# Optimization experiments

Hardware: AMD Instinct MI355X
Metric: run time of the kernel (lower is better)

The kernel has to match this reference:

```python
import jax, jax.numpy as jnp
import numpy as np

B, L, D, N_ORIG, GD, K_TARGET = 8, 512, 1024, 8192, 64, 256
_PI, _PJ = np.triu_indices(L, k=1)  # all global pairs i<j, shared across batch


def setup_inputs() -> dict:
    key = jax.random.key(0)
    k1, k2, k3 = jax.random.split(key, 3)
    x = jax.random.normal(k1, (B, L, D), jnp.float32)
    source = jax.random.uniform(k2, (B, L, N_ORIG), jnp.float32)
    W = jax.random.normal(k3, (GD, D), jnp.float32) * 0.02  # group_proj weight (out,in), no bias
    return {"x": x, "source": source, "W": W, "target_len": K_TARGET}


def _merge_single(x, s, W, r_step, pi, pj):
    # x: (S,D), s: (S,N). One greedy global merge step (r_step = S//2 >= r_total).
    S = x.shape[0]
    g = x @ W.T                                   # (S, GD)
    gn = jnp.linalg.norm(g, axis=-1)              # token weights (g.norm)
    gu = g / jnp.maximum(gn, 1e-12)[:, None]      # F.normalize(g, dim=-1)
    sim = (gu[pi] * gu[pj]).sum(-1)               # (P,) cosine sim of each pair
    # deterministic order: (-sim, i, j); lexsort's last key is primary
    order = jnp.lexsort((pj, pi, -sim))
    si = pi[order]
    sj = pj[order]

    # sequential greedy disjoint (mutual-exclusion) selection
    def body(carry, ij):
        partner, isj, cnt = carry
        i, j = ij
        used_i = (partner[i] >= 0) | isj[i]
        used_j = (partner[j] >= 0) | isj[j]
        sel = (~used_i) & (~used_j) & (cnt < r_step)
        partner = partner.at[i].set(jnp.where(sel, j, partner[i]))
        isj = isj.at[j].set(isj[j] | sel)
        return (partner, isj, cnt + sel.astype(jnp.int32)), None

    init = (jnp.full((S,), -1, jnp.int32), jnp.zeros((S,), bool), jnp.int32(0))
    (partner, isj, _), _ = jax.lax.scan(body, init, (si, sj))

    # kept tokens (everything not a merged-away j), in original order; greedy on a
    # complete graph always selects exactly r_step pairs, so K = S - r_step is static
    K = S - r_step
    keep = jnp.argsort(isj.astype(jnp.int32), stable=True)[:K]  # (K,)
    pk = partner[keep]
    has_p = pk >= 0
    pjx = jnp.where(has_p, pk, keep)  # safe partner index
    wi = gn[keep]
    wj = gn[pjx]
    tot = wi + wj + 1e-8
    xm = jnp.where(has_p[:, None], (wi[:, None] * x[keep] + wj[:, None] * x[pjx]) / tot[:, None], x[keep])
    sm = jnp.where(has_p[:, None], s[keep] + s[pjx], s[keep])
    return xm, sm


def reference(x, source, W, target_len):
    Bb, Ll, Dd = x.shape
    r_total = Ll - target_len
    if r_total <= 0:
        return x, source
    # with target_len = L//2, r_total <= floor(L/2): single greedy step (faithful)
    r_step = min(r_total, Ll // 2)
    pi = jnp.asarray(_PI, jnp.int32)
    pj = jnp.asarray(_PJ, jnp.int32)
    f = lambda xb, sb: _merge_single(xb, sb, W, r_step, pi, pj)
    return jax.vmap(f)(x, source)
```

## Files before the change

### kernel.cpp

```cpp
#include <hip/hip_runtime.h>

#define B_ 8
#define L_ 512
#define D_ 1024
#define N_ 8192
#define GD_ 64
#define K_ 256

#define XQ(q) ((q) ^ (((q) >> 4) & 7))

__global__ __launch_bounds__(256) void wt_kernel(const float* __restrict__ W,
                                                 float* __restrict__ Wt) {
  int idx = blockIdx.x * 256 + threadIdx.x;
  int d = idx >> 6, g = idx & 63;
  Wt[idx] = W[(size_t)g * D_ + d];
}

__global__ __launch_bounds__(256) void gproj_kernel(const float* __restrict__ x,
                                                    const float* __restrict__ Wt,
                                                    float* __restrict__ gu,
                                                    float* __restrict__ gn) {
  __shared__ __align__(16) float xs[16 * 1024];
  __shared__ __align__(16) float red[16][16][64];
  int blk = blockIdx.x;
  int b = blk >> 5;
  int t0 = (blk & 31) * 16;
  int tid = threadIdx.x;
  const float* xb = x + ((size_t)b * L_ + t0) * D_;
  for (int r = 0; r < 16; ++r) {
    int idx = r * 256 + tid;
    int tok = idx >> 8, q = idx & 255;
    float4 v = *(const float4*)(xb + (size_t)tok * D_ + q * 4);
    *(float4*)&xs[tok * 1024 + XQ(q) * 4] = v;
  }
  __syncthreads();
  int dq = tid & 15, kg = tid >> 4;
  float acc[16][4];
#pragma unroll
  for (int t = 0; t < 16; ++t)
#pragma unroll
    for (int d = 0; d < 4; ++d) acc[t][d] = 0.f;
  const float* wbase = Wt + (size_t)(kg * 64) * GD_ + dq * 4;
#pragma unroll 1
  for (int sub = 0; sub < 4; ++sub) {
    float4 wv[16];
#pragma unroll
    for (int kk = 0; kk < 16; ++kk)
      wv[kk] = *(const float4*)(wbase + (size_t)(sub * 16 + kk) * GD_);
#pragma unroll
    for (int tok = 0; tok < 16; ++tok) {
      float4 xv[4];
#pragma unroll
      for (int kq = 0; kq < 4; ++kq) {
        int q = kg * 16 + sub * 4 + kq;
        xv[kq] = *(const float4*)&xs[tok * 1024 + XQ(q) * 4];
      }
#pragma unroll
      for (int kq = 0; kq < 4; ++kq) {
        float xc[4] = {xv[kq].x, xv[kq].y, xv[kq].z, xv[kq].w};
#pragma unroll
        for (int c = 0; c < 4; ++c) {
          float4 w = wv[kq * 4 + c];
          acc[tok][0] += xc[c] * w.x;
          acc[tok][1] += xc[c] * w.y;
          acc[tok][2] += xc[c] * w.z;
          acc[tok][3] += xc[c] * w.w;
        }
      }
    }
  }
#pragma unroll
  for (int tok = 0; tok < 16; ++tok) {
    float4 p;
    p.x = acc[tok][0]; p.y = acc[tok][1]; p.z = acc[tok][2]; p.w = acc[tok][3];
    *(float4*)&red[kg][tok][dq * 4] = p;
  }
  __syncthreads();
  int tok = tid >> 4, dqo = tid & 15;
  float g[4] = {0.f, 0.f, 0.f, 0.f};
#pragma unroll
  for (int k = 0; k < 16; ++k) {
    float4 p = *(const float4*)&red[k][tok][dqo * 4];
    g[0] += p.x; g[1] += p.y; g[2] += p.z; g[3] += p.w;
  }
  double ss = 0.0;
#pragma unroll
  for (int d = 0; d < 4; ++d) ss += (double)g[d] * (double)g[d];
#pragma unroll
  for (int off = 1; off < 16; off <<= 1) ss += __shfl_xor(ss, off);
  float gnv = (float)sqrt(ss);
  float dn = fmaxf(gnv, 1e-12f);
  int t = t0 + tok;
  if (dqo == 0) gn[(size_t)b * L_ + t] = gnv;
  float4 o;
  o.x = g[0] / dn; o.y = g[1] / dn; o.z = g[2] / dn; o.w = g[3] / dn;
  *(float4*)(gu + ((size_t)b * L_ + t) * GD_ + dqo * 4) = o;
}

__global__ __launch_bounds__(256) void sim_kernel(const float* __restrict__ gu,
                                                  float* __restrict__ simo) {
  __shared__ __align__(16) float BsT[GD_][36];
  int b = blockIdx.z;
  int i0 = blockIdx.y * 32, j0 = blockIdx.x * 32;
  const float* gb = gu + (size_t)b * L_ * GD_;
  int tid = threadIdx.x;
  for (int f = tid; f < 32 * GD_; f += 256) {
    int r = f >> 6, k = f & 63;
    BsT[k][r] = gb[(size_t)(j0 + r) * GD_ + k];
  }
  int r = tid >> 3, c4 = (tid & 7) * 4;
  float af[GD_];
  const float4* arow = (const float4*)(gb + (size_t)(i0 + r) * GD_);
#pragma unroll
  for (int q = 0; q < 16; ++q) *(float4*)&af[q * 4] = arow[q];
  __syncthreads();
  double a0 = 0, a1 = 0, a2 = 0, a3 = 0;
#pragma unroll
  for (int k = 0; k < GD_; ++k) {
    double a = (double)af[k];
    float4 bv = *(const float4*)&BsT[k][c4];
    a0 += a * (double)bv.x;
    a1 += a * (double)bv.y;
    a2 += a * (double)bv.z;
    a3 += a * (double)bv.w;
  }
  float4 o;
  o.x = (float)a0; o.y = (float)a1; o.z = (float)a2; o.w = (float)a3;
  *(float4*)(simo + (size_t)b * L_ * L_ + (size_t)(i0 + r) * L_ + (j0 + c4)) = o;
}

__global__ __launch_bounds__(256) void topk_kernel(const float* __restrict__ sim,
                                                   unsigned long long* __restrict__ cand) {
  int wid = blockIdx.x * 4 + (threadIdx.x >> 6);
  int b = wid >> 9;
  int a = wid & 511;
  int lane = threadIdx.x & 63;
  const float* row = sim + ((size_t)b * L_ + a) * L_;
  int c0 = lane * 8;
  float4 v0 = *(const float4*)(row + c0);
  float4 v1 = *(const float4*)(row + c0 + 4);
  float vv[8] = {v0.x, v0.y, v0.z, v0.w, v1.x, v1.y, v1.z, v1.w};
  unsigned long long k[8];
#pragma unroll
  for (int s = 0; s < 8; ++s) {
    int bb = c0 + s;
    if (bb == a) {
      k[s] = 0;
    } else {
      unsigned u = __float_as_uint(vv[s]);
      u = (u & 0x80000000u) ? ~u : (u | 0x80000000u);
      int i = a < bb ? a : bb, j = a < bb ? bb : a;
      k[s] = ((unsigned long long)u << 18) |
             (unsigned long long)(0x3FFFFu - (((unsigned)i << 9) | (unsigned)j));
    }
  }
  unsigned long long* out = cand + ((size_t)b * L_ + a) * 16;
#pragma unroll
  for (int pass = 0; pass < 16; ++pass) {
    unsigned long long m = k[0];
#pragma unroll
    for (int s = 1; s < 8; ++s) m = k[s] > m ? k[s] : m;
#pragma unroll
    for (int off = 32; off; off >>= 1) {
      unsigned long long o = __shfl_xor(m, off);
      if (o > m) m = o;
    }
#pragma unroll
    for (int s = 0; s < 8; ++s)
      if (k[s] == m) k[s] = 0;
    if (lane == 0) out[pass] = m;
  }
}

__global__ __launch_bounds__(512) void match_kernel(const float* __restrict__ sim,
                                                    const unsigned long long* __restrict__ cand,
                                                    int* __restrict__ keepI,
                                                    int* __restrict__ keepJ) {
  int b = blockIdx.x;
  const float* S = sim + (size_t)b * L_ * L_;
  const unsigned long long* C = cand + (size_t)b * L_ * 16;
  __shared__ unsigned long long candL[L_][16];
  __shared__ unsigned long long bestkey[L_];
  __shared__ short partner[L_];
  __shared__ short liveA[L_], liveB[L_], rescanQ[L_];
  __shared__ unsigned char liveF[L_], needs[L_], head[L_];
  __shared__ int nLiveNew, nQ;
  int tid = threadIdx.x;
  int wave = tid >> 6, lane = tid & 63;
  for (int f = tid; f < L_ * 8; f += 512)
    ((ulonglong2*)candL)[f] = ((const ulonglong2*)C)[f];
  if (tid < L_) {
    partner[tid] = -1;
    liveF[tid] = 1;
    needs[tid] = 1;
    head[tid] = 0;
    liveA[tid] = (short)tid;
    bestkey[tid] = 0ull;
  }
  if (tid == 0) {
    nLiveNew = L_;
    nQ = 0;
  }
  __syncthreads();
  for (int round = 0; round < 300; ++round) {
    int nLive = nLiveNew;
    if (nLive == 0) break;
    short* cur = (round & 1) ? liveB : liveA;
    short* nxt = (round & 1) ? liveA : liveB;
    for (int idx = tid; idx < nLive; idx += 512) {
      int a = cur[idx];
      if (needs[a]) {
        int h = head[a];
        unsigned long long bk = 0ull;
        while (h < 16) {
          unsigned long long key = candL[a][h];
          if (key) {
            unsigned pk = 0x3FFFFu - (unsigned)(key & 0x3FFFFull);
            int i = (int)(pk >> 9), j = (int)(pk & 511u);
            int p = (i == a) ? j : i;
            if (liveF[p]) { bk = key; break; }
          }
          ++h;
        }
        head[a] = (unsigned char)h;
        if (bk) {
          bestkey[a] = bk;
          needs[a] = 0;
        } else {
          int q = atomicAdd(&nQ, 1);
          rescanQ[q] = (short)a;
        }
      }
    }
    __syncthreads();
    int nq = nQ;
    for (int q = wave; q < nq; q += 8) {
      int a = rescanQ[q];
      unsigned long long mk = 0ull;
      for (int kk = lane; kk < nLive; kk += 64) {
        int bb = cur[kk];
        if (bb != a) {
          float sv = S[(size_t)a * L_ + bb];
          unsigned u = __float_as_uint(sv);
          u = (u & 0x80000000u) ? ~u : (u | 0x80000000u);
          int i = a < bb ? a : bb, j = a < bb ? bb : a;
          unsigned long long key =
              ((unsigned long long)u << 18) |
              (unsigned long long)(0x3FFFFu - (((unsigned)i << 9) | (unsigned)j));
          if (key > mk) mk = key;
        }
      }
#pragma unroll
      for (int off = 32; off; off >>= 1) {
        unsigned long long o = __shfl_xor(mk, off);
        if (o > mk) mk = o;
      }
      if (lane == 0) {
        bestkey[a] = mk;
        needs[a] = 0;
      }
    }
    if (tid == 0) nLiveNew = 0;
    __syncthreads();
    for (int idx = tid; idx < nLive; idx += 512) {
      int a = cur[idx];
      unsigned pk = 0x3FFFFu - (unsigned)(bestkey[a] & 0x3FFFFull);
      int i = (int)(pk >> 9), j = (int)(pk & 511u);
      int p = (i == a) ? j : i;
      unsigned pk2 = 0x3FFFFu - (unsigned)(bestkey[p] & 0x3FFFFull);
      int i2 = (int)(pk2 >> 9), j2 = (int)(pk2 & 511u);
      int p2 = (i2 == p) ? j2 : i2;
      if (p2 == a) {
        partner[a] = (short)p;
        liveF[a] = 0;
      }
    }
    __syncthreads();
    for (int idx = tid; idx < nLive; idx += 512) {
      int a = cur[idx];
      if (liveF[a]) {
        unsigned pk = 0x3FFFFu - (unsigned)(bestkey[a] & 0x3FFFFull);
        int i = (int)(pk >> 9), j = (int)(pk & 511u);
        int p = (i == a) ? j : i;
        if (!liveF[p]) needs[a] = 1;
        int pos = atomicAdd(&nLiveNew, 1);
        nxt[pos] = (short)a;
      }
    }
    if (tid == 0) nQ = 0;
    __syncthreads();
  }
  if (wave == 0) {
    int base = 0;
    for (int c = 0; c < 8; ++c) {
      int a = c * 64 + lane;
      bool kept = partner[a] > a;
      unsigned long long m = __ballot(kept);
      int pos = base + (int)__popcll(m & ((1ull << lane) - 1ull));
      if (kept) {
        keepI[b * K_ + pos] = a;
        keepJ[b * K_ + pos] = partner[a];
      }
      base += (int)__popcll(m);
    }
  }
}

__global__ __launch_bounds__(256) void merge_kernel(const float* __restrict__ x,
                                                    const float* __restrict__ s,
                                                    const float* __restrict__ gn,
                                                    const int* __restrict__ keepI,
                                                    const int* __restrict__ keepJ,
                                                    float* __restrict__ xm,
                                                    float* __restrict__ sm) {
  int row = blockIdx.x;
  int b = row >> 8;
  int i = keepI[row], j = keepJ[row];
  float wi = gn[(size_t)b * L_ + i], wj = gn[(size_t)b * L_ + j];
  float tot = wi + wj + 1e-8f;
  int t = threadIdx.x;
  {
    const float4* xi = (const float4*)(x + ((size_t)b * L_ + i) * D_);
    const float4* xj = (const float4*)(x + ((size_t)b * L_ + j) * D_);
    float4* o = (float4*)(xm + (size_t)row * D_);
    float4 a = xi[t], c = xj[t];
    float4 r;
    r.x = (wi * a.x + wj * c.x) / tot;
    r.y = (wi * a.y + wj * c.y) / tot;
    r.z = (wi * a.z + wj * c.z) / tot;
    r.w = (wi * a.w + wj * c.w) / tot;
    o[t] = r;
  }
  {
    const float4* si = (const float4*)(s + ((size_t)b * L_ + i) * N_);
    const float4* sj = (const float4*)(s + ((size_t)b * L_ + j) * N_);
    float4* o = (float4*)(sm + (size_t)row * N_);
    for (int tt = t; tt < N_ / 4; tt += 256) {
      float4 a = si[tt], c = sj[tt];
      float4 r;
      r.x = a.x + c.x;
      r.y = a.y + c.y;
      r.z = a.z + c.z;
      r.w = a.w + c.w;
      o[tt] = r;
    }
  }
}

extern "C" void kernel_launch(void* const* d_in, const int* in_sizes, int n_in,
                              void* d_out, int out_size, void* d_ws, size_t ws_size,
                              hipStream_t stream) {
  (void)in_sizes; (void)n_in; (void)out_size; (void)ws_size;
  const float* x = (const float*)d_in[0];
  const float* src = (const float*)d_in[1];
  const float* W = (const float*)d_in[2];

  float* ws = (float*)d_ws;
  float* Wt = ws;
  float* gu = Wt + 65536;
  float* gn = gu + (size_t)B_ * L_ * GD_;
  float* sim = gn + (size_t)B_ * L_;
  int* keepI = (int*)(sim + (size_t)B_ * L_ * L_);
  int* keepJ = keepI + B_ * K_;
  unsigned long long* cand = (unsigned long long*)(keepJ + B_ * K_);

  float* xm = (float*)d_out;
  float* sm = xm + (size_t)B_ * K_ * D_;

  wt_kernel<<<256, 256, 0, stream>>>(W, Wt);
  gproj_kernel<<<256, 256, 0, stream>>>(x, Wt, gu, gn);
  sim_kernel<<<dim3(16, 16, 8), 256, 0, stream>>>(gu, sim);
  topk_kernel<<<1024, 256, 0, stream>>>(sim, cand);
  match_kernel<<<B_, 512, 0, stream>>>(sim, cand, keepI, keepJ);
  merge_kernel<<<B_ * K_, 256, 0, stream>>>(x, src, gn, keepI, keepJ, xm, sm);
}
```

Measured before the change: 311.5 us.

## Fuse similarity and top-k, deepen candidate lists, cut match syncs, split merge

Fuses the similarity GEMM and the per-row top-k candidate extraction into one kernel. Each block computes 16 full rows in shared memory, so top-k reads from LDS instead of re-reading the global sim matrix. Candidate depth grows from 16 to 24 to reduce expensive full-row rescans in the greedy matcher. The matcher uses double-buffered counters, which removes one barrier per round and skips the rescan barrier when no rescans are queued. The merge kernel is split into two blocks per output row for more parallelism. The fused kernel launches only 256 blocks with a serial j-loop, so it has less parallelism than before, and the deeper top-k adds more passes.

```diff
diff --git a/kernel.cpp b/kernel.cpp
--- a/kernel.cpp
+++ b/kernel.cpp
@@ -6,6 +6,7 @@
 #define N_ 8192
 #define GD_ 64
 #define K_ 256
+#define CD_ 24
 
 #define XQ(q) ((q) ^ (((q) >> 4) & 7))
 
@@ -97,78 +98,82 @@
   *(float4*)(gu + ((size_t)b * L_ + t) * GD_ + dqo * 4) = o;
 }
 
-__global__ __launch_bounds__(256) void sim_kernel(const float* __restrict__ gu,
-                                                  float* __restrict__ simo) {
-  __shared__ __align__(16) float BsT[GD_][36];
-  int b = blockIdx.z;
-  int i0 = blockIdx.y * 32, j0 = blockIdx.x * 32;
+__global__ __launch_bounds__(256) void sim_topk_kernel(const float* __restrict__ gu,
+                                                       float* __restrict__ simo,
+                                                       unsigned long long* __restrict__ cand) {
+  __shared__ __align__(16) float simL[16][512];
+  __shared__ __align__(16) float BsT[64][68];
+  int b = blockIdx.y;
+  int i0 = blockIdx.x * 16;
   const float* gb = gu + (size_t)b * L_ * GD_;
   int tid = threadIdx.x;
-  for (int f = tid; f < 32 * GD_; f += 256) {
-    int r = f >> 6, k = f & 63;
-    BsT[k][r] = gb[(size_t)(j0 + r) * GD_ + k];
-  }
-  int r = tid >> 3, c4 = (tid & 7) * 4;
+  int r = tid >> 4, c4 = (tid & 15) * 4;
   float af[GD_];
   const float4* arow = (const float4*)(gb + (size_t)(i0 + r) * GD_);
 #pragma unroll
   for (int q = 0; q < 16; ++q) *(float4*)&af[q * 4] = arow[q];
-  __syncthreads();
-  double a0 = 0, a1 = 0, a2 = 0, a3 = 0;
-#pragma unroll
-  for (int k = 0; k < GD_; ++k) {
-    double a = (double)af[k];
-    float4 bv = *(const float4*)&BsT[k][c4];
-    a0 += a * (double)bv.x;
-    a1 += a * (double)bv.y;
-    a2 += a * (double)bv.z;
-    a3 += a * (double)bv.w;
-  }
-  float4 o;
-  o.x = (float)a0; o.y = (float)a1; o.z = (float)a2; o.w = (float)a3;
-  *(float4*)(simo + (size_t)b * L_ * L_ + (size_t)(i0 + r) * L_ + (j0 + c4)) = o;
-}
-
-__global__ __launch_bounds__(256) void topk_kernel(const float* __restrict__ sim,
-                                                   unsigned long long* __restrict__ cand) {
-  int wid = blockIdx.x * 4 + (threadIdx.x >> 6);
-  int b = wid >> 9;
-  int a = wid & 511;
-  int lane = threadIdx.x & 63;
-  const float* row = sim + ((size_t)b * L_ + a) * L_;
-  int c0 = lane * 8;
-  float4 v0 = *(const float4*)(row + c0);
-  float4 v1 = *(const float4*)(row + c0 + 4);
-  float vv[8] = {v0.x, v0.y, v0.z, v0.w, v1.x, v1.y, v1.z, v1.w};
-  unsigned long long k[8];
-#pragma unroll
-  for (int s = 0; s < 8; ++s) {
-    int bb = c0 + s;
-    if (bb == a) {
-      k[s] = 0;
-    } else {
-      unsigned u = __float_as_uint(vv[s]);
-      u = (u & 0x80000000u) ? ~u : (u | 0x80000000u);
-      int i = a < bb ? a : bb, j = a < bb ? bb : a;
-      k[s] = ((unsigned long long)u << 18) |
-             (unsigned long long)(0x3FFFFu - (((unsigned)i << 9) | (unsigned)j));
-    }
-  }
-  unsigned long long* out = cand + ((size_t)b * L_ + a) * 16;
-#pragma unroll
-  for (int pass = 0; pass < 16; ++pass) {
-    unsigned long long m = k[0];
-#pragma unroll
-    for (int s = 1; s < 8; ++s) m = k[s] > m ? k[s] : m;
-#pragma unroll
-    for (int off = 32; off; off >>= 1) {
-      unsigned long long o = __shfl_xor(m, off);
-      if (o > m) m = o;
-    }
-#pragma unroll
-    for (int s = 0; s < 8; ++s)
-      if (k[s] == m) k[s] = 0;
-    if (lane == 0) out[pass] = m;
+  float* sgl = simo + (size_t)b * L_ * L_;
+#pragma unroll 1
+  for (int jt = 0; jt < 8; ++jt) {
+    int j0 = jt * 64;
+    for (int f = tid; f < 64 * GD_; f += 256) {
+      int br = f >> 6, k = f & 63;
+      BsT[k][br] = gb[(size_t)(j0 + br) * GD_ + k];
+    }
+    __syncthreads();
+    double a0 = 0, a1 = 0, a2 = 0, a3 = 0;
+#pragma unroll
+    for (int k = 0; k < GD_; ++k) {
+      double a = (double)af[k];
+      float4 bv = *(const float4*)&BsT[k][c4];
+      a0 += a * (double)bv.x;
+      a1 += a * (double)bv.y;
+      a2 += a * (double)bv.z;
+      a3 += a * (double)bv.w;
+    }
+    float4 o;
+    o.x = (float)a0; o.y = (float)a1; o.z = (float)a2; o.w = (float)a3;
+    *(float4*)&simL[r][j0 + c4] = o;
+    *(float4*)(sgl + (size_t)(i0 + r) * L_ + (j0 + c4)) = o;
+    __syncthreads();
+  }
+  int wave = tid >> 6, lane = tid & 63;
+  for (int rr = wave; rr < 16; rr += 4) {
+    int a = i0 + rr;
+    int c0 = lane * 8;
+    float vv[8];
+#pragma unroll
+    for (int s = 0; s < 8; ++s) vv[s] = simL[rr][c0 + s];
+    unsigned long long k[8];
+#pragma unroll
+    for (int s = 0; s < 8; ++s) {
+      int bb = c0 + s;
+      if (bb == a) {
+        k[s] = 0;
+      } else {
+        unsigned u = __float_as_uint(vv[s]);
+        u = (u & 0x80000000u) ? ~u : (u | 0x80000000u);
+        int i = a < bb ? a : bb, j = a < bb ? bb : a;
+        k[s] = ((unsigned long long)u << 18) |
+               (unsigned long long)(0x3FFFFu - (((unsigned)i << 9) | (unsigned)j));
+      }
+    }
+    unsigned long long* out = cand + ((size_t)b * L_ + a) * CD_;
+#pragma unroll 1
+    for (int pass = 0; pass < CD_; ++pass) {
+      unsigned long long m = k[0];
+#pragma unroll
+      for (int s = 1; s < 8; ++s) m = k[s] > m ? k[s] : m;
+#pragma unroll
+      for (int off = 32; off; off >>= 1) {
+        unsigned long long o = __shfl_xor(m, off);
+        if (o > m) m = o;
+      }
+#pragma unroll
+      for (int s = 0; s < 8; ++s)
+        if (k[s] == m) k[s] = 0;
+      if (lane == 0) out[pass] = m;
+    }
   }
 }
 
@@ -178,16 +183,16 @@
                                                     int* __restrict__ keepJ) {
   int b = blockIdx.x;
   const float* S = sim + (size_t)b * L_ * L_;
-  const unsigned long long* C = cand + (size_t)b * L_ * 16;
-  __shared__ unsigned long long candL[L_][16];
+  const unsigned long long* C = cand + (size_t)b * L_ * CD_;
+  __shared__ unsigned long long candL[L_][CD_];
   __shared__ unsigned long long bestkey[L_];
   __shared__ short partner[L_];
   __shared__ short liveA[L_], liveB[L_], rescanQ[L_];
   __shared__ unsigned char liveF[L_], needs[L_], head[L_];
-  __shared__ int nLiveNew, nQ;
+  __shared__ int cnt[2], nQ[2];
   int tid = threadIdx.x;
   int wave = tid >> 6, lane = tid & 63;
-  for (int f = tid; f < L_ * 8; f += 512)
+  for (int f = tid; f < L_ * (CD_ / 2); f += 512)
     ((ulonglong2*)candL)[f] = ((const ulonglong2*)C)[f];
   if (tid < L_) {
     partner[tid] = -1;
@@ -198,21 +203,26 @@
     bestkey[tid] = 0ull;
   }
   if (tid == 0) {
-    nLiveNew = L_;
-    nQ = 0;
+    cnt[0] = L_; cnt[1] = 0;
+    nQ[0] = 0; nQ[1] = 0;
   }
   __syncthreads();
   for (int round = 0; round < 300; ++round) {
-    int nLive = nLiveNew;
+    int par = round & 1;
+    int nLive = cnt[par];
     if (nLive == 0) break;
-    short* cur = (round & 1) ? liveB : liveA;
-    short* nxt = (round & 1) ? liveA : liveB;
+    short* cur = par ? liveB : liveA;
+    short* nxt = par ? liveA : liveB;
+    if (tid == 0) {
+      cnt[par ^ 1] = 0;
+      nQ[par ^ 1] = 0;
+    }
     for (int idx = tid; idx < nLive; idx += 512) {
       int a = cur[idx];
       if (needs[a]) {
         int h = head[a];
         unsigned long long bk = 0ull;
-        while (h < 16) {
+        while (h < CD_) {
           unsigned long long key = candL[a][h];
           if (key) {
             unsigned pk = 0x3FFFFu - (unsigned)(key & 0x3FFFFull);
@@ -227,41 +237,42 @@
           bestkey[a] = bk;
           needs[a] = 0;
         } else {
-          int q = atomicAdd(&nQ, 1);
+          int q = atomicAdd(&nQ[par], 1);
           rescanQ[q] = (short)a;
         }
       }
     }
     __syncthreads();
-    int nq = nQ;
-    for (int q = wave; q < nq; q += 8) {
-      int a = rescanQ[q];
-      unsigned long long mk = 0ull;
-      for (int kk = lane; kk < nLive; kk += 64) {
-        int bb = cur[kk];
-        if (bb != a) {
-          float sv = S[(size_t)a * L_ + bb];
-          unsigned u = __float_as_uint(sv);
-          u = (u & 0x80000000u) ? ~u : (u | 0x80000000u);
-          int i = a < bb ? a : bb, j = a < bb ? bb : a;
-          unsigned long long key =
-              ((unsigned long long)u << 18) |
-              (unsigned long long)(0x3FFFFu - (((unsigned)i << 9) | (unsigned)j));
-          if (key > mk) mk = key;
-        }
-      }
-#pragma unroll
-      for (int off = 32; off; off >>= 1) {
-        unsigned long long o = __shfl_xor(mk, off);
-        if (o > mk) mk = o;
-      }
-      if (lane == 0) {
-        bestkey[a] = mk;
-        needs[a] = 0;
-      }
-    }
-    if (tid == 0) nLiveNew = 0;
-    __syncthreads();
+    int nq = nQ[par];
+    if (nq > 0) {
+      for (int q = wave; q < nq; q += 8) {
+        int a = rescanQ[q];
+        unsigned long long mk = 0ull;
+        for (int kk = lane; kk < nLive; kk += 64) {
+          int bb = cur[kk];
+          if (bb != a) {
+            float sv = S[(size_t)a * L_ + bb];
+            unsigned u = __float_as_uint(sv);
+            u = (u & 0x80000000u) ? ~u : (u | 0x80000000u);
+            int i = a < bb ? a : bb, j = a < bb ? bb : a;
+            unsigned long long key =
+                ((unsigned long long)u << 18) |
+                (unsigned long long)(0x3FFFFu - (((unsigned)i << 9) | (unsigned)j));
+            if (key > mk) mk = key;
+          }
+        }
+#pragma unroll
+        for (int off = 32; off; off >>= 1) {
+          unsigned long long o = __shfl_xor(mk, off);
+          if (o > mk) mk = o;
+        }
+        if (lane == 0) {
+          bestkey[a] = mk;
+          needs[a] = 0;
+        }
+      }
+      __syncthreads();
+    }
     for (int idx = tid; idx < nLive; idx += 512) {
       int a = cur[idx];
       unsigned pk = 0x3FFFFu - (unsigned)(bestkey[a] & 0x3FFFFull);
@@ -283,11 +294,10 @@
         int i = (int)(pk >> 9), j = (int)(pk & 511u);
         int p = (i == a) ? j : i;
         if (!liveF[p]) needs[a] = 1;
-        int pos = atomicAdd(&nLiveNew, 1);
+        int pos = atomicAdd(&cnt[par ^ 1], 1);
         nxt[pos] = (short)a;
       }
     }
-    if (tid == 0) nQ = 0;
     __syncthreads();
   }
   if (wave == 0) {
@@ -313,13 +323,14 @@
                                                     const int* __restrict__ keepJ,
                                                     float* __restrict__ xm,
                                                     float* __restrict__ sm) {
-  int row = blockIdx.x;
+  int blk = blockIdx.x;
+  int row = blk >> 1, half = blk & 1;
   int b = row >> 8;
   int i = keepI[row], j = keepJ[row];
-  float wi = gn[(size_t)b * L_ + i], wj = gn[(size_t)b * L_ + j];
-  float tot = wi + wj + 1e-8f;
   int t = threadIdx.x;
-  {
+  if (half == 0) {
+    float wi = gn[(size_t)b * L_ + i], wj = gn[(size_t)b * L_ + j];
+    float tot = wi + wj + 1e-8f;
     const float4* xi = (const float4*)(x + ((size_t)b * L_ + i) * D_);
     const float4* xj = (const float4*)(x + ((size_t)b * L_ + j) * D_);
     float4* o = (float4*)(xm + (size_t)row * D_);
@@ -332,10 +343,11 @@
     o[t] = r;
   }
   {
-    const float4* si = (const float4*)(s + ((size_t)b * L_ + i) * N_);
-    const float4* sj = (const float4*)(s + ((size_t)b * L_ + j) * N_);
-    float4* o = (float4*)(sm + (size_t)row * N_);
-    for (int tt = t; tt < N_ / 4; tt += 256) {
+    size_t off = (size_t)half * (N_ / 2);
+    const float4* si = (const float4*)(s + ((size_t)b * L_ + i) * N_ + off);
+    const float4* sj = (const float4*)(s + ((size_t)b * L_ + j) * N_ + off);
+    float4* o = (float4*)(sm + (size_t)row * N_ + off);
+    for (int tt = t; tt < N_ / 8; tt += 256) {
       float4 a = si[tt], c = sj[tt];
       float4 r;
       r.x = a.x + c.x;
@@ -369,8 +381,7 @@
 
   wt_kernel<<<256, 256, 0, stream>>>(W, Wt);
   gproj_kernel<<<256, 256, 0, stream>>>(x, Wt, gu, gn);
-  sim_kernel<<<dim3(16, 16, 8), 256, 0, stream>>>(gu, sim);
-  topk_kernel<<<1024, 256, 0, stream>>>(sim, cand);
+  sim_topk_kernel<<<dim3(32, 8), 256, 0, stream>>>(gu, sim, cand);
   match_kernel<<<B_, 512, 0, stream>>>(sim, cand, keepI, keepJ);
-  merge_kernel<<<B_ * K_, 256, 0, stream>>>(x, src, gn, keepI, keepJ, xm, sm);
-}
+  merge_kernel<<<B_ * K_ * 2, 256, 0, stream>>>(x, src, gn, keepI, keepJ, xm, sm);
+}
```

Result: slower. 358.8 us (+15.2%).
